# Kernel optimization log

Hardware: AMD Instinct MI355X
Metric: run time of the kernel (lower is better)

Reference implementation:

```python
import jax, jax.numpy as jnp
from jax import lax
import numpy as np

B, DIM, H, W = 4, 256, 64, 64
C2 = 2 * DIM          # 512 internal channels
CB = DIM              # 256 channels per branch
NH = 8                # heads per branch (num_heads*2 // 2)
HD = CB // NH         # 32 head dim
SPLIT = 8
SCALE = HD ** -0.5
EPS = 1e-5


def layernorm(x, g, b):
    mu = jnp.mean(x, axis=-1, keepdims=True)
    var = jnp.mean(jnp.square(x - mu), axis=-1, keepdims=True)
    return (x - mu) * lax.rsqrt(var + EPS) * g + b


def lepe_branch(q, k, v, cw, cb, H_sp, W_sp):
    # q,k,v: [B, L, CB]; cross-shaped stripe-window attention with LePE
    nH, nW = H // H_sp, W // W_sp
    win = H_sp * W_sp

    def to_win(t):
        t = t.reshape(B, nH, H_sp, nW, W_sp, CB).transpose(0, 1, 3, 2, 4, 5)
        return t.reshape(B * nH * nW, win, NH, HD).transpose(0, 2, 1, 3)

    qw = to_win(q) * SCALE
    kw = to_win(k)
    # v as per-window images for depthwise LePE conv: [B*nH*nW, CB, H_sp, W_sp]
    v_img = v.reshape(B, nH, H_sp, nW, W_sp, CB).transpose(0, 1, 3, 5, 2, 4)
    v_img = v_img.reshape(B * nH * nW, CB, H_sp, W_sp)
    lepe = lax.conv_general_dilated(v_img, cw, (1, 1), 'SAME',
                                    feature_group_count=CB,
                                    dimension_numbers=('NCHW', 'OIHW', 'NCHW'))
    lepe = lepe + cb[None, :, None, None]
    vw = v_img.reshape(-1, NH, HD, win).transpose(0, 1, 3, 2)
    lepew = lepe.reshape(-1, NH, HD, win).transpose(0, 1, 3, 2)

    attn = jax.nn.softmax(jnp.einsum('bhid,bhjd->bhij', qw, kw), axis=-1)
    o = jnp.einsum('bhij,bhjd->bhid', attn, vw) + lepew
    # windows back to image token order: [B, H*W, CB]
    o = o.transpose(0, 2, 1, 3).reshape(B, nH, nW, H_sp, W_sp, CB)
    o = o.transpose(0, 1, 3, 2, 4, 5).reshape(B, H * W, CB)
    return o


def setup_inputs() -> dict:
    key = jax.random.key(0)
    ks = jax.random.split(key, 12)
    s = 0.02
    return {
        'x': jax.random.normal(ks[0], (B, DIM, H, W), jnp.float32),
        'w_embed': jax.random.normal(ks[1], (DIM, C2), jnp.float32) * s,
        'g1': 1.0 + jax.random.normal(ks[2], (C2,), jnp.float32) * s,
        'b1': jax.random.normal(ks[3], (C2,), jnp.float32) * s,
        'w_qkv': jax.random.normal(ks[4], (C2, 3 * C2), jnp.float32) * s,
        'conv_w0': jax.random.normal(ks[5], (CB, 1, 3, 3), jnp.float32) * s,
        'conv_b0': jax.random.normal(ks[6], (CB,), jnp.float32) * s,
        'conv_w1': jax.random.normal(ks[7], (CB, 1, 3, 3), jnp.float32) * s,
        'conv_b1': jax.random.normal(ks[8], (CB,), jnp.float32) * s,
        'w_proj': jax.random.normal(ks[9], (C2, C2), jnp.float32) * s,
        'b_proj': jax.random.normal(ks[10], (C2,), jnp.float32) * s,
        'w_out': jax.random.normal(ks[11], (C2, DIM), jnp.float32) * s,
    }


def reference(x, w_embed, g1, b1, w_qkv, conv_w0, conv_b0, conv_w1, conv_b1,
              w_proj, b_proj, w_out):
    L = H * W
    # b c h w -> b (h w) c, then embed to 2*dim
    xt = x.reshape(B, DIM, L).transpose(0, 2, 1)
    x2 = xt @ w_embed                          # [B, L, 512]
    img = layernorm(x2, g1, b1)
    qkv = (img @ w_qkv).reshape(B, L, 3, C2).transpose(2, 0, 1, 3)  # [3,B,L,512]
    q, k, v = qkv[0], qkv[1], qkv[2]
    # branch 0: horizontal stripes (H_sp=H, W_sp=split); branch 1: transpose
    o0 = lepe_branch(q[..., :CB], k[..., :CB], v[..., :CB], conv_w0, conv_b0, H, SPLIT)
    o1 = lepe_branch(q[..., CB:], k[..., CB:], v[..., CB:], conv_w1, conv_b1, SPLIT, W)
    att = jnp.concatenate([o0, o1], axis=2) @ w_proj + b_proj
    xo = x2 + att
    out = (xo @ w_out).transpose(0, 2, 1).reshape(B, DIM, H, W)
    vout = (v @ w_out).transpose(0, 2, 1).reshape(B, DIM, H, W)
    return out, vout
```

## Files before the change

kernel.cpp:

```cpp
#include <hip/hip_runtime.h>
#include <cstdint>

#define Bn 4
#define DIMn 256
#define Ln 4096
#define C2n 512
#define CBn 256
#define HDn 32
#define Mtot (Bn * Ln)

using bf16x8 = __attribute__((ext_vector_type(8))) short;
using f32x4 = __attribute__((ext_vector_type(4))) float;

static constexpr float kScale = 0.17677669529663687f;
static constexpr float kEps = 1e-5f;
static constexpr float kExpC = 0.17677669529663687f * 1.4426950408889634f;

__device__ __forceinline__ ushort f2bf(float f) {
  union {
    float f;
    unsigned u;
  } v;
  v.f = f;
  unsigned r = v.u + 0x7FFFu + ((v.u >> 16) & 1u);
  return (ushort)(r >> 16);
}

__device__ __forceinline__ float bf2f(ushort u) {
  union {
    unsigned u;
    float f;
  } v;
  v.u = (unsigned)u << 16;
  return v.f;
}

__device__ __forceinline__ unsigned cvtpk(float lo, float hi) {
  unsigned r;
  asm("v_cvt_pk_bf16_f32 %0, %1, %2" : "=v"(r) : "v"(lo), "v"(hi));
  return r;
}

__device__ __forceinline__ void gload16(const void* g, void* l) {
  __builtin_amdgcn_global_load_lds(
      (const __attribute__((address_space(1))) unsigned*)g,
      (__attribute__((address_space(3))) unsigned*)l, 16, 0, 0);
}

enum { G_EMBED = 0, G_QKV = 1, G_PROJ = 2 };

template <int MODE, int ND, int KD, int LDB>
__global__ __launch_bounds__(256) void gemm_bf(
    const ushort* __restrict__ A, const ushort* __restrict__ Bt,
    const ushort* __restrict__ resid, const float* __restrict__ bias,
    ushort* __restrict__ aux) {
  constexpr int NT = ND / 128;
  __shared__ ushort As[128 * 64];
  __shared__ ushort Bs[128 * 64];

  const int tid = threadIdx.x;
  const int wid = tid >> 6;
  const int lane = tid & 63;
  const int m0 = (blockIdx.x / NT) * 128;
  const int n0 = (blockIdx.x % NT) * 128;

  const int gs = (wid < 2) ? KD : LDB;
  const ushort* gsrc = (wid < 2)
                           ? A + (size_t)(m0 + (wid & 1) * 64) * KD
                           : Bt + (size_t)(n0 + (wid & 1) * 64) * LDB;
  ushort* lbase = (wid < 2 ? As : Bs) + (wid & 1) * (64 * 64);
  const int r8 = lane >> 3;
  const int c8 = lane & 7;

  f32x4 acc[4][4];
#pragma unroll
  for (int i = 0; i < 4; ++i)
#pragma unroll
    for (int j = 0; j < 4; ++j) acc[i][j] = (f32x4){0.f, 0.f, 0.f, 0.f};

  const int wm = (wid & 1) * 64;
  const int wn = (wid >> 1) * 64;
  const int lr = lane & 15;
  const int kq = lane >> 4;

  for (int k0 = 0; k0 < KD; k0 += 64) {
    __syncthreads();
#pragma unroll
    for (int i = 0; i < 8; ++i) {
      const ushort* g = gsrc + (size_t)(i * 8 + r8) * gs + (k0 + c8 * 8);
      gload16(g, lbase + i * 512);
    }
    __syncthreads();
#pragma unroll
    for (int kk = 0; kk < 2; ++kk) {
      bf16x8 af[4], bfr[4];
#pragma unroll
      for (int i = 0; i < 4; ++i)
        af[i] = *(const bf16x8*)(As + (wm + i * 16 + lr) * 64 +
                                 (kk * 4 + kq) * 8);
#pragma unroll
      for (int j = 0; j < 4; ++j)
        bfr[j] = *(const bf16x8*)(Bs + (wn + j * 16 + lr) * 64 +
                                  (kk * 4 + kq) * 8);
#pragma unroll
      for (int i = 0; i < 4; ++i)
#pragma unroll
        for (int j = 0; j < 4; ++j)
          acc[i][j] = __builtin_amdgcn_mfma_f32_16x16x32_bf16(
              af[i], bfr[j], acc[i][j], 0, 0, 0);
    }
  }

#pragma unroll
  for (int i = 0; i < 4; ++i) {
#pragma unroll
    for (int j = 0; j < 4; ++j) {
#pragma unroll
      for (int t = 0; t < 4; ++t) {
        const int mr = m0 + wm + i * 16 + kq * 4 + t;
        const int nc = n0 + wn + j * 16 + lr;
        float val = acc[i][j][t];
        if constexpr (MODE == G_EMBED) {
          aux[(size_t)mr * 512 + nc] = f2bf(val);
        } else if constexpr (MODE == G_QKV) {
          if (nc < 512) val *= kExpC;
          aux[(size_t)mr * 1536 + nc] = f2bf(val);
        } else {
          const float v2 =
              val + bf2f(resid[(size_t)mr * 512 + nc]) + bias[nc];
          aux[(size_t)mr * 512 + nc] = f2bf(v2);
        }
      }
    }
  }
}

__global__ __launch_bounds__(256) void gemm_out2(
    const ushort* __restrict__ A, const ushort* __restrict__ Bt0,
    const ushort* __restrict__ Bt1, float* __restrict__ C) {
  constexpr int KD = 512;
  constexpr int NT = Mtot / 128;
  __shared__ ushort As[128 * 64];
  __shared__ ushort Bs[128 * 64];

  const int sel = blockIdx.x >> 8;
  const int bid = blockIdx.x & 255;
  const ushort* Bt = sel ? Bt1 : Bt0;
  const int ldb = sel ? 1536 : 512;
  const size_t outBase = sel ? (size_t)Bn * DIMn * Ln : 0;

  const int tid = threadIdx.x;
  const int wid = tid >> 6;
  const int lane = tid & 63;
  const int m0 = (bid / NT) * 128;
  const int n0 = (bid % NT) * 128;

  const int gs = (wid < 2) ? KD : ldb;
  const ushort* gsrc = (wid < 2)
                           ? A + (size_t)(m0 + (wid & 1) * 64) * KD
                           : Bt + (size_t)(n0 + (wid & 1) * 64) * ldb;
  ushort* lbase = (wid < 2 ? As : Bs) + (wid & 1) * (64 * 64);
  const int r8 = lane >> 3;
  const int c8 = lane & 7;

  f32x4 acc[4][4];
#pragma unroll
  for (int i = 0; i < 4; ++i)
#pragma unroll
    for (int j = 0; j < 4; ++j) acc[i][j] = (f32x4){0.f, 0.f, 0.f, 0.f};

  const int wm = (wid & 1) * 64;
  const int wn = (wid >> 1) * 64;
  const int lr = lane & 15;
  const int kq = lane >> 4;

  for (int k0 = 0; k0 < KD; k0 += 64) {
    __syncthreads();
#pragma unroll
    for (int i = 0; i < 8; ++i) {
      const ushort* g = gsrc + (size_t)(i * 8 + r8) * gs + (k0 + c8 * 8);
      gload16(g, lbase + i * 512);
    }
    __syncthreads();
#pragma unroll
    for (int kk = 0; kk < 2; ++kk) {
      bf16x8 af[4], bfr[4];
#pragma unroll
      for (int i = 0; i < 4; ++i)
        af[i] = *(const bf16x8*)(As + (wm + i * 16 + lr) * 64 +
                                 (kk * 4 + kq) * 8);
#pragma unroll
      for (int j = 0; j < 4; ++j)
        bfr[j] = *(const bf16x8*)(Bs + (wn + j * 16 + lr) * 64 +
                                  (kk * 4 + kq) * 8);
#pragma unroll
      for (int i = 0; i < 4; ++i)
#pragma unroll
        for (int j = 0; j < 4; ++j)
          acc[i][j] = __builtin_amdgcn_mfma_f32_16x16x32_bf16(
              af[i], bfr[j], acc[i][j], 0, 0, 0);
    }
  }

#pragma unroll
  for (int i = 0; i < 4; ++i)
#pragma unroll
    for (int j = 0; j < 4; ++j)
#pragma unroll
      for (int t = 0; t < 4; ++t) {
        const int mr = m0 + wm + i * 16 + kq * 4 + t;
        const int nc = n0 + wn + j * 16 + lr;
        C[outBase + ((size_t)(nc >> 12)) * ((size_t)DIMn * Ln) +
          (size_t)mr * Ln + (nc & 4095)] = acc[i][j][t];
      }
}

__global__ __launch_bounds__(256) void cvt_wall(
    const float* __restrict__ w_embed, const float* __restrict__ w_qkv,
    const float* __restrict__ w_proj, const float* __restrict__ w_out,
    ushort* __restrict__ we_t, ushort* __restrict__ wq_t,
    ushort* __restrict__ wp_t, ushort* __restrict__ wo_t) {
  const int blk = blockIdx.x;
  const float* in;
  ushort* out;
  int lgK, N, t;
  if (blk < 512) {
    in = w_embed; out = we_t; lgK = 8; N = 512; t = blk * 256 + threadIdx.x;
  } else if (blk < 3584) {
    in = w_qkv; out = wq_t; lgK = 9; N = 1536;
    t = (blk - 512) * 256 + threadIdx.x;
  } else if (blk < 4608) {
    in = w_proj; out = wp_t; lgK = 9; N = 512;
    t = (blk - 3584) * 256 + threadIdx.x;
  } else {
    in = w_out; out = wo_t; lgK = 9; N = 256;
    t = (blk - 4608) * 256 + threadIdx.x;
  }
  const int K = 1 << lgK;
  const int n = t >> lgK;
  const int k = t & (K - 1);
  out[t] = f2bf(in[(size_t)k * N + n]);
}

__global__ __launch_bounds__(256) void cvt_x(const float* __restrict__ x,
                                             ushort* __restrict__ xe) {
  __shared__ ushort tile[64][65];
  const int blk = blockIdx.x;
  const int lt = blk & 63;
  const int ct = (blk >> 6) & 3;
  const int b = blk >> 8;
  const int l0 = lt * 64, c0 = ct * 64;
  const int t = threadIdx.x;
  const int lanel = t & 63;
  const int grp = t >> 6;
#pragma unroll
  for (int it = 0; it < 16; ++it) {
    const int c = grp * 16 + it;
    tile[c][lanel] =
        f2bf(x[(size_t)b * (DIMn * Ln) + (size_t)(c0 + c) * Ln + l0 + lanel]);
  }
  __syncthreads();
#pragma unroll
  for (int it = 0; it < 16; ++it) {
    const int l = grp * 16 + it;
    xe[((size_t)b * Ln + l0 + l) * 256 + c0 + lanel] = tile[lanel][l];
  }
}

__global__ __launch_bounds__(128) void ln_fuse(const ushort* __restrict__ x2,
                                               const float* __restrict__ g1,
                                               const float* __restrict__ b1,
                                               ushort* __restrict__ xln) {
  const int row = blockIdx.x;
  const int t = threadIdx.x;
  const ushort4 u4 = *(const ushort4*)&x2[(size_t)row * 512 + t * 4];
  float v[4] = {bf2f(u4.x), bf2f(u4.y), bf2f(u4.z), bf2f(u4.w)};
  float s = v[0] + v[1] + v[2] + v[3];
  float s2 = v[0] * v[0] + v[1] * v[1] + v[2] * v[2] + v[3] * v[3];
#pragma unroll
  for (int off = 32; off > 0; off >>= 1) {
    s += __shfl_down(s, off);
    s2 += __shfl_down(s2, off);
  }
  __shared__ float red[4];
  if ((t & 63) == 0) {
    red[t >> 6] = s;
    red[2 + (t >> 6)] = s2;
  }
  __syncthreads();
  const float S = red[0] + red[1];
  const float S2 = red[2] + red[3];
  const float mu = S * (1.f / 512.f);
  const float rs = rsqrtf(S2 * (1.f / 512.f) - mu * mu + kEps);
  const float4 g = *(const float4*)&g1[t * 4];
  const float4 bb = *(const float4*)&b1[t * 4];
  ushort4 o;
  o.x = f2bf((v[0] - mu) * rs * g.x + bb.x);
  o.y = f2bf((v[1] - mu) * rs * g.y + bb.y);
  o.z = f2bf((v[2] - mu) * rs * g.z + bb.z);
  o.w = f2bf((v[3] - mu) * rs * g.w + bb.w);
  *(ushort4*)&xln[(size_t)row * 512 + t * 4] = o;
}

__global__ __launch_bounds__(256, 4) void attn_m(
    const ushort* __restrict__ qkv, ushort* __restrict__ obf,
    const float* __restrict__ cw0, const float* __restrict__ cb0,
    const float* __restrict__ cw1, const float* __restrict__ cb1) {
  __shared__ ushort VtS[32 * 520];
  __shared__ ushort KsS[32 * 40];
  __shared__ float denS[4 * 64];
  __shared__ float cwS[288];
  __shared__ float cbS[32];

  const int blk = blockIdx.x;
  const int branch = blk >> 9;
  const int b = (blk >> 7) & 3;
  const int win = (blk >> 4) & 7;
  const int head = (blk >> 1) & 7;
  const int qh = blk & 1;
  const int tid = threadIdx.x;
  const int w = tid >> 6;
  const int lane = tid & 63;
  const int lr = lane & 15;
  const int kq = lane >> 4;
  const int qcol = branch * CBn + head * HDn;

  const float* cw = branch ? cw1 : cw0;
  const float* cb = branch ? cb1 : cb0;
  for (int i = tid; i < 288; i += 256) cwS[i] = cw[head * 288 + i];
  if (tid < 32) cbS[tid] = cb[head * 32 + tid];

  auto tok2l = [&](int p) -> int {
    return branch == 0 ? ((p >> 3) * 64 + win * 8 + (p & 7)) : (win * 512 + p);
  };
  const size_t rowbase = (size_t)b * Ln;

#pragma unroll
  for (int rr = 0; rr < 2; ++rr) {
    const int j = tid + rr * 256;
    const ushort* vrow = qkv + (rowbase + tok2l(j)) * 1536 + 1024 + qcol;
#pragma unroll
    for (int g = 0; g < 4; ++g) {
      const bf16x8 u = *(const bf16x8*)(vrow + g * 8);
#pragma unroll
      for (int e = 0; e < 8; ++e)
        VtS[(g * 8 + e) * 520 + j] = (ushort)u[e];
    }
  }

  bf16x8 qf[4];
#pragma unroll
  for (int qt = 0; qt < 4; ++qt) {
    const int p = qh * 256 + w * 64 + qt * 16 + lr;
    qf[qt] =
        *(const bf16x8*)(qkv + (rowbase + tok2l(p)) * 1536 + qcol + kq * 8);
  }

  f32x4 acc[4][2];
#pragma unroll
  for (int qt = 0; qt < 4; ++qt) {
    acc[qt][0] = (f32x4){0.f, 0.f, 0.f, 0.f};
    acc[qt][1] = (f32x4){0.f, 0.f, 0.f, 0.f};
  }
  float den[4] = {};
  const f32x4 zero4 = (f32x4){0.f, 0.f, 0.f, 0.f};

  for (int kt = 0; kt < 16; ++kt) {
    const int k0 = kt * 32;
    __syncthreads();
    {
      const int j = tid >> 3;
      const int d0 = (tid & 7) * 4;
      const int row = ((j >> 2) & 1) * 16 + (j >> 3) * 4 + (j & 3);
      const ushort4 k4 = *(const ushort4*)(qkv +
                                           (rowbase + tok2l(k0 + j)) * 1536 +
                                           512 + qcol + d0);
      *(ushort4*)&KsS[row * 40 + d0] = k4;
    }
    __syncthreads();

    const bf16x8 kf0 = *(const bf16x8*)&KsS[lr * 40 + kq * 8];
    const bf16x8 kf1 = *(const bf16x8*)&KsS[(16 + lr) * 40 + kq * 8];
    const bf16x8 vf0 = *(const bf16x8*)&VtS[lr * 520 + k0 + kq * 8];
    const bf16x8 vf1 = *(const bf16x8*)&VtS[(16 + lr) * 520 + k0 + kq * 8];

#pragma unroll
    for (int qt = 0; qt < 4; ++qt) {
      const f32x4 s0 =
          __builtin_amdgcn_mfma_f32_16x16x32_bf16(kf0, qf[qt], zero4, 0, 0, 0);
      const f32x4 s1 =
          __builtin_amdgcn_mfma_f32_16x16x32_bf16(kf1, qf[qt], zero4, 0, 0, 0);
      float e0[4], e1[4];
#pragma unroll
      for (int t = 0; t < 4; ++t) {
        e0[t] = __builtin_amdgcn_exp2f(s0[t]);
        e1[t] = __builtin_amdgcn_exp2f(s1[t]);
      }
      den[qt] += (e0[0] + e0[1] + e0[2] + e0[3]) +
                 (e1[0] + e1[1] + e1[2] + e1[3]);
      union {
        unsigned u[4];
        bf16x8 v;
      } pa;
      pa.u[0] = cvtpk(e0[0], e0[1]);
      pa.u[1] = cvtpk(e0[2], e0[3]);
      pa.u[2] = cvtpk(e1[0], e1[1]);
      pa.u[3] = cvtpk(e1[2], e1[3]);
      acc[qt][0] = __builtin_amdgcn_mfma_f32_16x16x32_bf16(pa.v, vf0,
                                                           acc[qt][0], 0, 0, 0);
      acc[qt][1] = __builtin_amdgcn_mfma_f32_16x16x32_bf16(pa.v, vf1,
                                                           acc[qt][1], 0, 0, 0);
    }
  }

#pragma unroll
  for (int qt = 0; qt < 4; ++qt) {
    float d = den[qt];
    d += __shfl_xor(d, 16);
    d += __shfl_xor(d, 32);
    if (lane < 16) denS[w * 64 + qt * 16 + lr] = d;
  }
  __syncthreads();

  const int Hs = branch ? 8 : 64;
  const int Ws = branch ? 64 : 8;
#pragma unroll
  for (int qt = 0; qt < 4; ++qt) {
#pragma unroll
    for (int t = 0; t < 4; ++t) {
      const int p = qh * 256 + w * 64 + qt * 16 + kq * 4 + t;
      const int l = tok2l(p);
      const int hl = branch ? (p >> 6) : (p >> 3);
      const int wl = branch ? (p & 63) : (p & 7);
      const float inv = 1.f / denS[w * 64 + qt * 16 + kq * 4 + t];
      ushort* orow = obf + ((size_t)b * Ln + l) * 512 + qcol;
#pragma unroll
      for (int dt = 0; dt < 2; ++dt) {
        const int d = dt * 16 + lr;
        float le = cbS[d];
#pragma unroll
        for (int dh = -1; dh <= 1; ++dh) {
          const int hh = hl + dh;
          if (hh < 0 || hh >= Hs) continue;
#pragma unroll
          for (int dw = -1; dw <= 1; ++dw) {
            const int ww = wl + dw;
            if (ww < 0 || ww >= Ws) continue;
            const int pp = hh * Ws + ww;
            le = fmaf(bf2f(VtS[d * 520 + pp]),
                      cwS[d * 9 + (dh + 1) * 3 + (dw + 1)], le);
          }
        }
        orow[d] = f2bf(fmaf(acc[qt][dt][t], inv, le));
      }
    }
  }
}

extern "C" void kernel_launch(void* const* d_in, const int* in_sizes, int n_in,
                              void* d_out, int out_size, void* d_ws,
                              size_t ws_size, hipStream_t stream) {
  const float* x = (const float*)d_in[0];
  const float* w_embed = (const float*)d_in[1];
  const float* g1 = (const float*)d_in[2];
  const float* b1 = (const float*)d_in[3];
  const float* w_qkv = (const float*)d_in[4];
  const float* cw0 = (const float*)d_in[5];
  const float* cb0 = (const float*)d_in[6];
  const float* cw1 = (const float*)d_in[7];
  const float* cb1 = (const float*)d_in[8];
  const float* w_proj = (const float*)d_in[9];
  const float* b_proj = (const float*)d_in[10];
  const float* w_out = (const float*)d_in[11];
  float* out = (float*)d_out;

  char* p = (char*)d_ws;
  ushort* x2bf = (ushort*)p;
  p += (size_t)Mtot * 512 * 2;
  ushort* qkvbf = (ushort*)p;
  p += (size_t)Mtot * 1536 * 2;
  ushort* xe = (ushort*)p;
  ushort* obf = (ushort*)p;
  p += (size_t)Mtot * 512 * 2;
  ushort* xln = (ushort*)p;
  ushort* xobf = (ushort*)p;
  p += (size_t)Mtot * 512 * 2;
  ushort* we_t = (ushort*)p;
  p += (size_t)512 * 256 * 2;
  ushort* wq_t = (ushort*)p;
  p += (size_t)1536 * 512 * 2;
  ushort* wp_t = (ushort*)p;
  p += (size_t)512 * 512 * 2;
  ushort* wo_t = (ushort*)p;

  cvt_wall<<<dim3(5120), 256, 0, stream>>>(w_embed, w_qkv, w_proj, w_out,
                                           we_t, wq_t, wp_t, wo_t);
  cvt_x<<<dim3(1024), 256, 0, stream>>>(x, xe);

  gemm_bf<G_EMBED, 512, 256, 256><<<dim3(128 * 4), 256, 0, stream>>>(
      xe, we_t, nullptr, nullptr, x2bf);
  ln_fuse<<<dim3(Mtot), 128, 0, stream>>>(x2bf, g1, b1, xln);
  gemm_bf<G_QKV, 1536, 512, 512><<<dim3(128 * 12), 256, 0, stream>>>(
      xln, wq_t, nullptr, nullptr, qkvbf);
  attn_m<<<dim3(1024), 256, 0, stream>>>(qkvbf, obf, cw0, cb0, cw1, cb1);
  gemm_bf<G_PROJ, 512, 512, 512><<<dim3(128 * 4), 256, 0, stream>>>(
      obf, wp_t, x2bf, b_proj, xobf);
  gemm_out2<<<dim3(512), 256, 0, stream>>>(wo_t, xobf, qkvbf + 1024, out);
}
```

Measured before the change: 173.1 us.

## Write QKV in per-window head-major layout and tile weight transpose

The QKV GEMM epilogue now scatters q, k and v into separate buffers laid out per branch/batch/window/head/token so attention reads contiguous 64-byte head rows instead of strided rows of a 1536-wide matrix. V is also written a second time in row-major form for the final output GEMM, which adds extra write traffic. The attention block index is remapped to interleave work across the grid, and the weight conversion kernel is rewritten as an LDS-tiled transpose for coalesced reads and writes. The epilogue scatter writes individual elements with scattered addresses, which may cost write efficiency.

After: 169.2 us. 1.02x faster.

```diff
diff --git a/kernel.cpp b/kernel.cpp
--- a/kernel.cpp
+++ b/kernel.cpp
@@ -53,7 +53,8 @@
 __global__ __launch_bounds__(256) void gemm_bf(
     const ushort* __restrict__ A, const ushort* __restrict__ Bt,
     const ushort* __restrict__ resid, const float* __restrict__ bias,
-    ushort* __restrict__ aux) {
+    ushort* __restrict__ aux, ushort* __restrict__ kp,
+    ushort* __restrict__ vp, ushort* __restrict__ vrow) {
   constexpr int NT = ND / 128;
   __shared__ ushort As[128 * 64];
   __shared__ ushort Bs[128 * 64];
@@ -119,12 +120,31 @@
       for (int t = 0; t < 4; ++t) {
         const int mr = m0 + wm + i * 16 + kq * 4 + t;
         const int nc = n0 + wn + j * 16 + lr;
-        float val = acc[i][j][t];
+        const float val = acc[i][j][t];
         if constexpr (MODE == G_EMBED) {
           aux[(size_t)mr * 512 + nc] = f2bf(val);
         } else if constexpr (MODE == G_QKV) {
-          if (nc < 512) val *= kExpC;
-          aux[(size_t)mr * 1536 + nc] = f2bf(val);
+          const int sect = nc >> 9;
+          const int c = nc & 511;
+          const int br = c >> 8;
+          const int hd = (c >> 5) & 7;
+          const int d = c & 31;
+          const int bb = mr >> 12;
+          const int l = mr & 4095;
+          const int win = br ? (l >> 9) : ((l >> 3) & 7);
+          const int pp = br ? (l & 511) : (((l >> 6) << 3) | (l & 7));
+          const size_t off =
+              (((((size_t)br * 4 + bb) * 8 + win) * 8 + hd) * 512 + pp) * 32 +
+              d;
+          if (sect == 0) {
+            aux[off] = f2bf(val * kExpC);
+          } else if (sect == 1) {
+            kp[off] = f2bf(val);
+          } else {
+            const ushort bv = f2bf(val);
+            vp[off] = bv;
+            vrow[(size_t)mr * 512 + c] = bv;
+          }
         } else {
           const float v2 =
               val + bf2f(resid[(size_t)mr * 512 + nc]) + bias[nc];
@@ -146,7 +166,6 @@
   const int sel = blockIdx.x >> 8;
   const int bid = blockIdx.x & 255;
   const ushort* Bt = sel ? Bt1 : Bt0;
-  const int ldb = sel ? 1536 : 512;
   const size_t outBase = sel ? (size_t)Bn * DIMn * Ln : 0;
 
   const int tid = threadIdx.x;
@@ -155,10 +174,9 @@
   const int m0 = (bid / NT) * 128;
   const int n0 = (bid % NT) * 128;
 
-  const int gs = (wid < 2) ? KD : ldb;
   const ushort* gsrc = (wid < 2)
                            ? A + (size_t)(m0 + (wid & 1) * 64) * KD
-                           : Bt + (size_t)(n0 + (wid & 1) * 64) * ldb;
+                           : Bt + (size_t)(n0 + (wid & 1) * 64) * KD;
   ushort* lbase = (wid < 2 ? As : Bs) + (wid & 1) * (64 * 64);
   const int r8 = lane >> 3;
   const int c8 = lane & 7;
@@ -178,7 +196,7 @@
     __syncthreads();
 #pragma unroll
     for (int i = 0; i < 8; ++i) {
-      const ushort* g = gsrc + (size_t)(i * 8 + r8) * gs + (k0 + c8 * 8);
+      const ushort* g = gsrc + (size_t)(i * 8 + r8) * KD + (k0 + c8 * 8);
       gload16(g, lbase + i * 512);
     }
     __syncthreads();
@@ -220,26 +238,36 @@
     const float* __restrict__ w_proj, const float* __restrict__ w_out,
     ushort* __restrict__ we_t, ushort* __restrict__ wq_t,
     ushort* __restrict__ wp_t, ushort* __restrict__ wo_t) {
+  __shared__ ushort tile[64][65];
   const int blk = blockIdx.x;
   const float* in;
   ushort* out;
-  int lgK, N, t;
-  if (blk < 512) {
-    in = w_embed; out = we_t; lgK = 8; N = 512; t = blk * 256 + threadIdx.x;
-  } else if (blk < 3584) {
-    in = w_qkv; out = wq_t; lgK = 9; N = 1536;
-    t = (blk - 512) * 256 + threadIdx.x;
-  } else if (blk < 4608) {
-    in = w_proj; out = wp_t; lgK = 9; N = 512;
-    t = (blk - 3584) * 256 + threadIdx.x;
+  int K, N, ti;
+  if (blk < 32) {
+    in = w_embed; out = we_t; K = 256; N = 512; ti = blk;
+  } else if (blk < 224) {
+    in = w_qkv; out = wq_t; K = 512; N = 1536; ti = blk - 32;
+  } else if (blk < 288) {
+    in = w_proj; out = wp_t; K = 512; N = 512; ti = blk - 224;
   } else {
-    in = w_out; out = wo_t; lgK = 9; N = 256;
-    t = (blk - 4608) * 256 + threadIdx.x;
-  }
-  const int K = 1 << lgK;
-  const int n = t >> lgK;
-  const int k = t & (K - 1);
-  out[t] = f2bf(in[(size_t)k * N + n]);
+    in = w_out; out = wo_t; K = 512; N = 256; ti = blk - 288;
+  }
+  const int ntN = N >> 6;
+  const int k0 = (ti / ntN) << 6;
+  const int n0 = (ti % ntN) << 6;
+  const int c = threadIdx.x & 63;
+  const int g = threadIdx.x >> 6;
+#pragma unroll
+  for (int it = 0; it < 16; ++it) {
+    const int r = it * 4 + g;
+    tile[r][c] = f2bf(in[(size_t)(k0 + r) * N + n0 + c]);
+  }
+  __syncthreads();
+#pragma unroll
+  for (int it = 0; it < 16; ++it) {
+    const int nn = it * 4 + g;
+    out[(size_t)(n0 + nn) * K + k0 + c] = tile[c][nn];
+  }
 }
 
 __global__ __launch_bounds__(256) void cvt_x(const float* __restrict__ x,
@@ -303,7 +331,8 @@
 }
 
 __global__ __launch_bounds__(256, 4) void attn_m(
-    const ushort* __restrict__ qkv, ushort* __restrict__ obf,
+    const ushort* __restrict__ qp, const ushort* __restrict__ kp,
+    const ushort* __restrict__ vp, ushort* __restrict__ obf,
     const float* __restrict__ cw0, const float* __restrict__ cb0,
     const float* __restrict__ cw1, const float* __restrict__ cb1) {
   __shared__ ushort VtS[32 * 520];
@@ -312,12 +341,12 @@
   __shared__ float cwS[288];
   __shared__ float cbS[32];
 
-  const int blk = blockIdx.x;
-  const int branch = blk >> 9;
-  const int b = (blk >> 7) & 3;
-  const int win = (blk >> 4) & 7;
-  const int head = (blk >> 1) & 7;
-  const int qh = blk & 1;
+  const int work = ((blockIdx.x & 7) << 7) | (blockIdx.x >> 3);
+  const int branch = work >> 9;
+  const int b = (work >> 7) & 3;
+  const int win = (work >> 4) & 7;
+  const int head = (work >> 1) & 7;
+  const int qh = work & 1;
   const int tid = threadIdx.x;
   const int w = tid >> 6;
   const int lane = tid & 63;
@@ -333,12 +362,13 @@
   auto tok2l = [&](int p) -> int {
     return branch == 0 ? ((p >> 3) * 64 + win * 8 + (p & 7)) : (win * 512 + p);
   };
-  const size_t rowbase = (size_t)b * Ln;
+  const size_t base =
+      (((((size_t)branch * 4 + b) * 8 + win) * 8 + head) * 512) * 32;
 
 #pragma unroll
   for (int rr = 0; rr < 2; ++rr) {
     const int j = tid + rr * 256;
-    const ushort* vrow = qkv + (rowbase + tok2l(j)) * 1536 + 1024 + qcol;
+    const ushort* vrow = vp + base + (size_t)j * 32;
 #pragma unroll
     for (int g = 0; g < 4; ++g) {
       const bf16x8 u = *(const bf16x8*)(vrow + g * 8);
@@ -352,8 +382,7 @@
 #pragma unroll
   for (int qt = 0; qt < 4; ++qt) {
     const int p = qh * 256 + w * 64 + qt * 16 + lr;
-    qf[qt] =
-        *(const bf16x8*)(qkv + (rowbase + tok2l(p)) * 1536 + qcol + kq * 8);
+    qf[qt] = *(const bf16x8*)(qp + base + (size_t)p * 32 + kq * 8);
   }
 
   f32x4 acc[4][2];
@@ -372,9 +401,8 @@
       const int j = tid >> 3;
       const int d0 = (tid & 7) * 4;
       const int row = ((j >> 2) & 1) * 16 + (j >> 3) * 4 + (j & 3);
-      const ushort4 k4 = *(const ushort4*)(qkv +
-                                           (rowbase + tok2l(k0 + j)) * 1536 +
-                                           512 + qcol + d0);
+      const ushort4 k4 =
+          *(const ushort4*)(kp + base + (size_t)(k0 + j) * 32 + d0);
       *(ushort4*)&KsS[row * 40 + d0] = k4;
     }
     __syncthreads();
@@ -477,14 +505,21 @@
   char* p = (char*)d_ws;
   ushort* x2bf = (ushort*)p;
   p += (size_t)Mtot * 512 * 2;
-  ushort* qkvbf = (ushort*)p;
-  p += (size_t)Mtot * 1536 * 2;
-  ushort* xe = (ushort*)p;
+  ushort* qp = (ushort*)p;
+  p += (size_t)Mtot * 512 * 2;
+  ushort* kp = (ushort*)p;
+  p += (size_t)Mtot * 512 * 2;
+  ushort* vp = (ushort*)p;
+  p += (size_t)Mtot * 512 * 2;
+  ushort* vrow = (ushort*)p;
+  p += (size_t)Mtot * 512 * 2;
   ushort* obf = (ushort*)p;
   p += (size_t)Mtot * 512 * 2;
   ushort* xln = (ushort*)p;
   ushort* xobf = (ushort*)p;
   p += (size_t)Mtot * 512 * 2;
+  ushort* xe = (ushort*)p;
+  p += (size_t)Mtot * 256 * 2;
   ushort* we_t = (ushort*)p;
   p += (size_t)512 * 256 * 2;
   ushort* wq_t = (ushort*)p;
@@ -493,17 +528,17 @@
   p += (size_t)512 * 512 * 2;
   ushort* wo_t = (ushort*)p;
 
-  cvt_wall<<<dim3(5120), 256, 0, stream>>>(w_embed, w_qkv, w_proj, w_out,
-                                           we_t, wq_t, wp_t, wo_t);
+  cvt_wall<<<dim3(320), 256, 0, stream>>>(w_embed, w_qkv, w_proj, w_out,
+                                          we_t, wq_t, wp_t, wo_t);
   cvt_x<<<dim3(1024), 256, 0, stream>>>(x, xe);
 
   gemm_bf<G_EMBED, 512, 256, 256><<<dim3(128 * 4), 256, 0, stream>>>(
-      xe, we_t, nullptr, nullptr, x2bf);
+      xe, we_t, nullptr, nullptr, x2bf, nullptr, nullptr, nullptr);
   ln_fuse<<<dim3(Mtot), 128, 0, stream>>>(x2bf, g1, b1, xln);
   gemm_bf<G_QKV, 1536, 512, 512><<<dim3(128 * 12), 256, 0, stream>>>(
-      xln, wq_t, nullptr, nullptr, qkvbf);
-  attn_m<<<dim3(1024), 256, 0, stream>>>(qkvbf, obf, cw0, cb0, cw1, cb1);
+      xln, wq_t, nullptr, nullptr, qp, kp, vp, vrow);
+  attn_m<<<dim3(1024), 256, 0, stream>>>(qp, kp, vp, obf, cw0, cb0, cw1, cb1);
   gemm_bf<G_PROJ, 512, 512, 512><<<dim3(128 * 4), 256, 0, stream>>>(
-      obf, wp_t, x2bf, b_proj, xobf);
-  gemm_out2<<<dim3(512), 256, 0, stream>>>(wo_t, xobf, qkvbf + 1024, out);
-}
+      obf, wp_t, x2bf, b_proj, xobf, nullptr, nullptr, nullptr);
+  gemm_out2<<<dim3(512), 256, 0, stream>>>(wo_t, xobf, vrow, out);
+}
```
